# Kernel tuning notes

Measured on AMD Instinct MI355X. Metric: run time of the kernel, lower is better.

## Reference

```python
import jax, jax.numpy as jnp
import numpy as np

THRESHOLD = 0.5
NEG_POS_RATIO = 3
ALPHA = 1.0
N_CLASSES = 81


def xy_to_cxcy(xy):
    return jnp.concatenate([(xy[..., :2] + xy[..., 2:]) / 2.0,
                            xy[..., 2:] - xy[..., :2]], axis=-1)


def cxcy_to_xy(cxcy):
    return jnp.concatenate([cxcy[..., :2] - cxcy[..., 2:] / 2.0,
                            cxcy[..., :2] + cxcy[..., 2:] / 2.0], axis=-1)


def cxcy_to_gcxgcy(cxcy, priors_cxcy):
    # SSD encoding with standard variances (0.1 for center, 0.2 for size)
    g_cxcy = (cxcy[..., :2] - priors_cxcy[..., :2]) / (priors_cxcy[..., 2:] / 10.0)
    g_wh = jnp.log(cxcy[..., 2:] / priors_cxcy[..., 2:]) * 5.0
    return jnp.concatenate([g_cxcy, g_wh], axis=-1)


def iou_pairwise(a_xy, b_xy):
    # a_xy: (N, O, 4), b_xy: (P, 4) -> (N, O, P)
    lt = jnp.maximum(a_xy[..., :, None, :2], b_xy[None, None, :, :2])
    rb = jnp.minimum(a_xy[..., :, None, 2:], b_xy[None, None, :, 2:])
    wh = jnp.clip(rb - lt, 0.0)
    inter = wh[..., 0] * wh[..., 1]
    area_a = (a_xy[..., 2] - a_xy[..., 0]) * (a_xy[..., 3] - a_xy[..., 1])
    area_b = (b_xy[:, 2] - b_xy[:, 0]) * (b_xy[:, 3] - b_xy[:, 1])
    union = area_a[..., :, None] + area_b[None, None, :] - inter
    return inter / union


def setup_inputs() -> dict:
    key = jax.random.key(0)
    k1, k2, k3, k4, k5, k6, k7 = jax.random.split(key, 7)
    N, P, C, O = 32, 8732, N_CLASSES, 16
    predicted_locs = jax.random.normal(k1, (N, P, 4), dtype=jnp.float32)
    predicted_scores = jax.random.normal(k2, (N, P, C), dtype=jnp.float32)
    # ground-truth boxes: build valid cxcy then convert to xy in [0, 1]
    b_cxy = jax.random.uniform(k3, (N, O, 2), minval=0.2, maxval=0.8)
    b_wh = jax.random.uniform(k4, (N, O, 2), minval=0.05, maxval=0.3)
    boxes = cxcy_to_xy(jnp.concatenate([b_cxy, b_wh], axis=-1)).astype(jnp.float32)
    labels = jax.random.randint(k5, (N, O), 1, C).astype(jnp.int32)  # 0 = background
    # priors in cxcy, valid (positive wh)
    p_cxy = jax.random.uniform(k6, (P, 2), minval=0.05, maxval=0.95)
    p_wh = jax.random.uniform(k7, (P, 2), minval=0.05, maxval=0.4)
    priors_cxcy = jnp.concatenate([p_cxy, p_wh], axis=-1).astype(jnp.float32)
    return {"predicted_locs": predicted_locs, "predicted_scores": predicted_scores,
            "boxes": boxes, "labels": labels, "priors_cxcy": priors_cxcy}


def reference(predicted_locs, predicted_scores, boxes, labels, priors_cxcy):
    N, P, C = predicted_scores.shape
    O = boxes.shape[1]
    priors_xy = cxcy_to_xy(priors_cxcy)  # (P, 4)

    overlap = iou_pairwise(boxes, priors_xy)            # (N, O, P)
    overlap_for_each_prior = overlap.max(axis=1)        # (N, P)
    object_for_each_prior = overlap.argmax(axis=1)      # (N, P)
    prior_for_each_object = overlap.argmax(axis=2)      # (N, O)

    obj_ids = jnp.arange(O)

    def assign(ofp, ovl, pfo):
        # force each object to be matched to its best prior with overlap 1
        ofp = ofp.at[pfo].set(obj_ids)
        ovl = ovl.at[pfo].set(1.0)
        return ofp, ovl

    object_for_each_prior, overlap_for_each_prior = jax.vmap(assign)(
        object_for_each_prior, overlap_for_each_prior, prior_for_each_object)

    label_for_each_prior = jnp.take_along_axis(labels, object_for_each_prior, axis=1)  # (N, P)
    true_classes = jnp.where(overlap_for_each_prior < THRESHOLD, 0, label_for_each_prior)

    matched_boxes = jnp.take_along_axis(
        boxes, object_for_each_prior[..., None], axis=1)  # (N, P, 4)
    true_locs = cxcy_to_gcxgcy(xy_to_cxcy(matched_boxes), priors_cxcy)

    positive = true_classes != 0                          # (N, P)
    pos_f = positive.astype(predicted_locs.dtype)

    # localization loss (L1, reduction='none' in original despite the name)
    loc_per_prior = jnp.abs(predicted_locs - true_locs).sum(axis=-1)  # (N, P)
    n_pos_total = pos_f.sum()
    loc_loss = (loc_per_prior * pos_f).sum() / (4.0 * n_pos_total)

    # confidence loss (cross entropy per prior)
    logp = jax.nn.log_softmax(predicted_scores, axis=-1)
    ce = -jnp.take_along_axis(logp, true_classes[..., None], axis=-1)[..., 0]  # (N, P)

    conf_loss_pos = (ce * pos_f).sum()
    ce_neg = jnp.where(positive, 0.0, ce)
    ce_neg_sorted = -jnp.sort(-ce_neg, axis=1)            # descending
    n_positives = positive.sum(axis=1)                    # (N,)
    hard = (jnp.arange(P)[None, :] < (NEG_POS_RATIO * n_positives)[:, None]).astype(ce.dtype)
    conf_loss_hard_neg = (ce_neg_sorted * hard).sum()
    conf_loss = (conf_loss_hard_neg + conf_loss_pos) / n_pos_total

    return conf_loss + ALPHA * loc_loss
```

## Files before the change

### kernel.cpp

```cpp
#include <hip/hip_runtime.h>
#include <hip/hip_bf16.h>
#include <stdint.h>

#define BLOCK 256
#define TPB 256
#define SROWS 128
#define MAXO 64
#define TK_THREADS 1024
#define CK_MAX 4096

__global__ void match_object_kernel(const float* __restrict__ boxes,
                                    const float* __restrict__ priors,
                                    int* __restrict__ pfop,
                                    float* __restrict__ acc, int* __restrict__ n_pos,
                                    unsigned* __restrict__ done, int N, int P, int O) {
    __shared__ unsigned long long swm[4];
    int idx = blockIdx.x, tid = threadIdx.x;
    if (idx == 0) {
        for (int j = tid; j < N; j += BLOCK) n_pos[j] = 0;
        if (tid >= 64 && tid < 67) acc[tid - 64] = 0.f;
        if (tid == 96) *done = 0u;
    }
    const float* b = boxes + (size_t)idx * 4;
    float bx0 = b[0], by0 = b[1], bx1 = b[2], by1 = b[3];
    float areaa = (bx1 - bx0) * (by1 - by0);

    unsigned long long best = 0ULL;
    for (int p = tid; p < P; p += BLOCK) {
        float4 pr = ((const float4*)priors)[p];
        float px0 = pr.x - pr.z * 0.5f, py0 = pr.y - pr.w * 0.5f;
        float px1 = pr.x + pr.z * 0.5f, py1 = pr.y + pr.w * 0.5f;
        float areab = (px1 - px0) * (py1 - py0);
        float ltx = fmaxf(bx0, px0), lty = fmaxf(by0, py0);
        float rbx = fminf(bx1, px1), rby = fminf(by1, py1);
        float wx = fmaxf(rbx - ltx, 0.f), wy = fmaxf(rby - lty, 0.f);
        float inter = wx * wy;
        float iou = inter / (areaa + areab - inter);
        unsigned long long cand = (((unsigned long long)__float_as_uint(iou)) << 32) |
                                  (unsigned long long)(0xFFFFFFFFu - (unsigned)p);
        if (cand > best) best = cand;
    }
    #pragma unroll
    for (int off = 32; off >= 1; off >>= 1) {
        unsigned long long other = __shfl_down(best, off);
        if (other > best) best = other;
    }
    if ((tid & 63) == 0) swm[tid >> 6] = best;
    __syncthreads();
    if (tid == 0) {
        unsigned long long r = swm[0];
        for (int w = 1; w < BLOCK / 64; ++w) if (swm[w] > r) r = swm[w];
        pfop[idx] = (int)(0xFFFFFFFFu - (unsigned)(r & 0xFFFFFFFFull));
    }
}

__global__ void __launch_bounds__(TPB)
fused_staged_kernel(const float* __restrict__ boxes,
                    const float* __restrict__ priors,
                    const float* __restrict__ locs,
                    const int* __restrict__ labels,
                    const int* __restrict__ pfop,
                    const float* __restrict__ scores,
                    float* __restrict__ ce_neg,
                    float* __restrict__ pb_loc, float* __restrict__ pb_pce,
                    int* __restrict__ pb_npos,
                    int N, int P, int O) {
    __shared__ float4 sstage4[SROWS * 81 / 4];
    __shared__ float sbx[MAXO * 4];
    __shared__ int   spf[MAXO];
    __shared__ int   slab[MAXO];
    __shared__ float sl[4], sp[4]; __shared__ int sn[4];
    const float* sstage = (const float*)sstage4;

    int n = blockIdx.y, bx = blockIdx.x, tid = threadIdx.x;
    int w = tid >> 6, lane = tid & 63;
    int p0 = bx * SROWS;
    int rows = P - p0; if (rows > SROWS) rows = SROWS;
    int p = p0 + tid;
    bool valid = tid < rows;
    size_t t = (size_t)n * P + p;

    for (int i = tid; i < O * 4; i += TPB) sbx[i] = boxes[(size_t)n * O * 4 + i];
    for (int i = tid; i < O; i += TPB) { spf[i] = pfop[n * O + i]; slab[i] = labels[n * O + i]; }
    float4 pr = make_float4(0.f, 0.f, 1.f, 1.f);
    float4 pl = make_float4(0.f, 0.f, 0.f, 0.f);
    if (valid) {
        pr = ((const float4*)priors)[p];
        pl = ((const float4*)locs)[t];
    }

    const float4* chunk = (const float4*)(scores + ((size_t)n * P + p0) * 81);
    if (rows == SROWS) {
        #pragma unroll
        for (int j = 0; j < 10; ++j)
            sstage4[j * TPB + tid] = chunk[j * TPB + tid];
        if (tid < 32)
            sstage4[10 * TPB + tid] = chunk[10 * TPB + tid];
    } else {
        int nf4 = rows * 81 / 4;
        for (int j = 0; j < 11; ++j) {
            int idx = j * TPB + tid;
            if (idx < nf4) sstage4[idx] = chunk[idx];
        }
    }
    __syncthreads();

    float my_loc = 0.f, my_pce = 0.f; int my_pos = 0;
    if (valid) {
        const float* row = sstage + tid * 81;
        float e = 0.f;
        #pragma unroll
        for (int j = 0; j < 81; ++j) e += __expf(row[j]);

        float px0 = pr.x - pr.z * 0.5f, py0 = pr.y - pr.w * 0.5f;
        float px1 = pr.x + pr.z * 0.5f, py1 = pr.y + pr.w * 0.5f;
        float areab = (px1 - px0) * (py1 - py0);
        float best = -1.f; int bo = 0;
        for (int o = 0; o < O; ++o) {
            float x0 = sbx[o*4+0], y0 = sbx[o*4+1], x1 = sbx[o*4+2], y1 = sbx[o*4+3];
            float ltx = fmaxf(x0, px0), lty = fmaxf(y0, py0);
            float rbx = fminf(x1, px1), rby = fminf(y1, py1);
            float wx = fmaxf(rbx - ltx, 0.f), wy = fmaxf(rby - lty, 0.f);
            float inter = wx * wy;
            float areao = (x1 - x0) * (y1 - y0);
            float iou = inter / (areao + areab - inter);
            if (iou > best) { best = iou; bo = o; }
        }
        int fo = -1;
        for (int o = 0; o < O; ++o) if (spf[o] == p) fo = o;
        int obj; float ov;
        if (fo >= 0) { obj = fo; ov = 1.0f; }
        else         { obj = bo; ov = best; }
        int tc = (ov < 0.5f) ? 0 : slab[obj];

        float stc = row[tc];
        float ce = logf(e) - stc;
        bool pos = (tc != 0);
        ce_neg[t] = pos ? 0.f : ce;
        if (pos) {
            my_pce = ce; my_pos = 1;
            float x0 = sbx[obj*4+0], y0 = sbx[obj*4+1], x1 = sbx[obj*4+2], y1 = sbx[obj*4+3];
            float cx = (x0 + x1) * 0.5f, cy = (y0 + y1) * 0.5f;
            float bw = x1 - x0, bh = y1 - y0;
            float g0 = (cx - pr.x) / (pr.z / 10.0f);
            float g1 = (cy - pr.y) / (pr.w / 10.0f);
            float g2 = logf(bw / pr.z) * 5.0f;
            float g3 = logf(bh / pr.w) * 5.0f;
            my_loc = fabsf(pl.x-g0) + fabsf(pl.y-g1) + fabsf(pl.z-g2) + fabsf(pl.w-g3);
        }
    }

    #pragma unroll
    for (int off = 32; off >= 1; off >>= 1) {
        my_loc += __shfl_down(my_loc, off);
        my_pce += __shfl_down(my_pce, off);
        my_pos += __shfl_down(my_pos, off);
    }
    if (lane == 0) { sl[w] = my_loc; sp[w] = my_pce; sn[w] = my_pos; }
    __syncthreads();
    if (tid == 0) {
        int npb = gridDim.x;
        pb_loc[n * npb + bx]  = (sl[0] + sl[1]) + (sl[2] + sl[3]);
        pb_pce[n * npb + bx]  = (sp[0] + sp[1]) + (sp[2] + sp[3]);
        pb_npos[n * npb + bx] = sn[0] + sn[1] + sn[2] + sn[3];
    }
}

__global__ void match_prior_kernel(const float* __restrict__ boxes,
                                   const float* __restrict__ priors,
                                   const float* __restrict__ locs,
                                   const int* __restrict__ labels,
                                   const int* __restrict__ pfop,
                                   int* __restrict__ tcarr,
                                   float* __restrict__ acc, int* __restrict__ n_pos,
                                   int N, int P, int O) {
    __shared__ float sbx[MAXO * 4];
    __shared__ float sarea[MAXO];
    __shared__ int   spf[MAXO];
    __shared__ int   slab[MAXO];
    int n = blockIdx.y, tid = threadIdx.x;
    if (tid < O * 4) sbx[tid] = boxes[(size_t)n * O * 4 + tid];
    if (tid >= 128 && tid < 128 + O) spf[tid - 128]  = pfop[n * O + (tid - 128)];
    if (tid >= 192 && tid < 192 + O) slab[tid - 192] = labels[n * O + (tid - 192)];
    __syncthreads();
    if (tid < O)
        sarea[tid] = (sbx[tid*4+2] - sbx[tid*4+0]) * (sbx[tid*4+3] - sbx[tid*4+1]);
    __syncthreads();

    int p = blockIdx.x * BLOCK + tid;
    bool valid = p < P;
    float my_loc = 0.f; int my_pos = 0;
    if (valid) {
        float4 pr = ((const float4*)priors)[p];
        float px0 = pr.x - pr.z * 0.5f, py0 = pr.y - pr.w * 0.5f;
        float px1 = pr.x + pr.z * 0.5f, py1 = pr.y + pr.w * 0.5f;
        float areab = (px1 - px0) * (py1 - py0);

        float best = -1.f; int bo = 0;
        for (int o = 0; o < O; ++o) {
            float ltx = fmaxf(sbx[o*4+0], px0);
            float lty = fmaxf(sbx[o*4+1], py0);
            float rbx = fminf(sbx[o*4+2], px1);
            float rby = fminf(sbx[o*4+3], py1);
            float wx = fmaxf(rbx - ltx, 0.f), wy = fmaxf(rby - lty, 0.f);
            float inter = wx * wy;
            float iou = inter / (sarea[o] + areab - inter);
            if (iou > best) { best = iou; bo = o; }
        }
        int fo = -1;
        for (int o = 0; o < O; ++o) if (spf[o] == p) fo = o;
        int obj; float ov;
        if (fo >= 0) { obj = fo; ov = 1.0f; }
        else         { obj = bo; ov = best; }
        int lab = slab[obj];
        int tc = (ov < 0.5f) ? 0 : lab;
        tcarr[(size_t)n * P + p] = tc;
        if (tc != 0) {
            my_pos = 1;
            float x0 = sbx[obj*4+0], y0 = sbx[obj*4+1], x1 = sbx[obj*4+2], y1 = sbx[obj*4+3];
            float cx = (x0 + x1) * 0.5f, cy = (y0 + y1) * 0.5f;
            float w = x1 - x0, h = y1 - y0;
            float g0 = (cx - pr.x) / (pr.z / 10.0f);
            float g1 = (cy - pr.y) / (pr.w / 10.0f);
            float g2 = logf(w / pr.z) * 5.0f;
            float g3 = logf(h / pr.w) * 5.0f;
            const float* pl = locs + ((size_t)n * P + p) * 4;
            my_loc = fabsf(pl[0]-g0) + fabsf(pl[1]-g1) + fabsf(pl[2]-g2) + fabsf(pl[3]-g3);
        }
    }
    #pragma unroll
    for (int off = 32; off >= 1; off >>= 1) {
        my_loc += __shfl_down(my_loc, off);
        my_pos += __shfl_down(my_pos, off);
    }
    if ((tid & 63) == 0 && my_pos) {
        atomicAdd(&acc[0], my_loc);
        atomicAdd(&n_pos[n], my_pos);
    }
}

__global__ void loss_generic_kernel(const float* __restrict__ scores,
                                    const int* __restrict__ tcarr,
                                    float* __restrict__ ce_neg, float* __restrict__ acc,
                                    int NP, int C) {
    int t = blockIdx.x * blockDim.x + threadIdx.x;
    if (t >= NP) return;
    int tc = tcarr[t];
    const float* s = scores + (size_t)t * C;
    float m = -3.0e38f;
    for (int j = 0; j < C; ++j) m = fmaxf(m, s[j]);
    float l = 0.f, stc = 0.f;
    for (int j = 0; j < C; ++j) {
        float v = s[j];
        l += __expf(v - m);
        if (j == tc) stc = v;
    }
    float ce = m + logf(l) - stc;
    bool pos = (tc != 0);
    ce_neg[t] = pos ? 0.f : ce;
    if (pos) atomicAdd(&acc[1], ce);
}

__global__ void topk_final_kernel(const float* __restrict__ ce_neg,
                                  int* __restrict__ n_pos,
                                  const float* __restrict__ pb_loc,
                                  const float* __restrict__ pb_pce,
                                  const int* __restrict__ pb_npos, int npb,
                                  float* __restrict__ acc, unsigned* __restrict__ done,
                                  int N, int P, unsigned* __restrict__ out) {
    __shared__ unsigned skeys[8732];
    __shared__ int hist[4096];
    __shared__ int part[1024];
    __shared__ int s_tb, s_ca, s_tb2, s_ca2, s_cnt, s_np;
    __shared__ float shf[16];
    int n = blockIdx.x, tid = threadIdx.x;

    int k;
    if (npb > 0) {
        if (tid < 64) {
            float psl = 0.f, psp = 0.f; int psn = 0;
            for (int i = tid; i < npb; i += 64) {
                psl += pb_loc[n * npb + i];
                psp += pb_pce[n * npb + i];
                psn += pb_npos[n * npb + i];
            }
            #pragma unroll
            for (int off = 32; off >= 1; off >>= 1) {
                psl += __shfl_down(psl, off);
                psp += __shfl_down(psp, off);
                psn += __shfl_down(psn, off);
            }
            if (tid == 0) {
                s_np = psn;
                n_pos[n] = psn;
                if (psl != 0.f) atomicAdd(&acc[0], psl);
                if (psp != 0.f) atomicAdd(&acc[1], psp);
            }
        }
        __syncthreads();
        k = 3 * s_np;
    } else {
        k = 3 * n_pos[n];
    }
    if (k > P) k = P;
    float bsum = 0.f;

    if (k > 0) {
        const float* row = ce_neg + (size_t)n * P;
        for (int i = tid; i < P; i += TK_THREADS) skeys[i] = __float_as_uint(row[i]);
        #pragma unroll
        for (int b = 0; b < 4; ++b) hist[tid * 4 + b] = 0;
        __syncthreads();

        for (int i = tid; i < P; i += TK_THREADS) atomicAdd(&hist[skeys[i] >> 20], 1);
        __syncthreads();
        int h0 = hist[tid*4], h1 = hist[tid*4+1], h2 = hist[tid*4+2], h3 = hist[tid*4+3];
        part[tid] = h0 + h1 + h2 + h3;
        __syncthreads();
        for (int s = 1; s < 1024; s <<= 1) {
            int v = part[tid] + ((tid + s < 1024) ? part[tid + s] : 0);
            __syncthreads();
            part[tid] = v;
            __syncthreads();
        }
        int sfx = (tid + 1 < 1024) ? part[tid + 1] : 0;
        int sf3 = sfx, sf2 = sfx + h3, sf1 = sf2 + h2, sf0 = sf1 + h1;
        if (sf0 < k && k <= sf0 + h0) { s_tb = tid*4;   s_ca = sf0; }
        if (sf1 < k && k <= sf1 + h1) { s_tb = tid*4+1; s_ca = sf1; }
        if (sf2 < k && k <= sf2 + h2) { s_tb = tid*4+2; s_ca = sf2; }
        if (sf3 < k && k <= sf3 + h3) { s_tb = tid*4+3; s_ca = sf3; }
        __syncthreads();
        int tb = s_tb, kk = k - s_ca;

        if (tid < 256) part[tid] = 0;
        __syncthreads();
        float ssum = 0.f;
        for (int i = tid; i < P; i += TK_THREADS) {
            unsigned key = skeys[i];
            int bin = key >> 20;
            if (bin > tb) ssum += __uint_as_float(key);
            else if (bin == tb) atomicAdd(&part[(key >> 12) & 255u], 1);
        }
        __syncthreads();
        if (tid < 256) {
            int cum = 0;
            for (int b = tid + 1; b < 256; ++b) cum += part[b];
            int h = part[tid];
            if (cum < kk && kk <= cum + h) { s_tb2 = tid; s_ca2 = cum; }
        }
        if (tid == 0) s_cnt = 0;
        __syncthreads();
        int tb2 = s_tb2, kk2 = kk - s_ca2;

        unsigned* ckeys = (unsigned*)hist;
        for (int i = tid; i < P; i += TK_THREADS) {
            unsigned key = skeys[i];
            if ((int)(key >> 20) == tb) {
                int b2 = (key >> 12) & 255u;
                if (b2 > tb2) ssum += __uint_as_float(key);
                else if (b2 == tb2) {
                    int slot = atomicAdd(&s_cnt, 1);
                    if (slot < CK_MAX) ckeys[slot] = key;
                }
            }
        }
        __syncthreads();
        int m = s_cnt; if (m > CK_MAX) m = CK_MAX;
        for (int i = tid; i < m; i += TK_THREADS) {
            unsigned key = ckeys[i];
            int rank = 0;
            for (int j = 0; j < m; ++j) {
                unsigned kj = ckeys[j];
                rank += (kj > key) || (kj == key && j < i);
            }
            if (rank < kk2) ssum += __uint_as_float(key);
        }
        #pragma unroll
        for (int off = 32; off >= 1; off >>= 1) ssum += __shfl_down(ssum, off);
        __syncthreads();
        if ((tid & 63) == 0) shf[tid >> 6] = ssum;
        __syncthreads();
        float tot = 0.f;
        for (int i = 0; i < 16; ++i) tot += shf[i];
        bsum = tot;
    }

    if (tid == 0) {
        if (bsum != 0.f) atomicAdd(&acc[2], bsum);
        __threadfence();
        unsigned old = atomicAdd(done, 1u);
        if (old == (unsigned)(N - 1)) {
            float a0 = atomicAdd(&acc[0], 0.f);
            float a1 = atomicAdd(&acc[1], 0.f);
            float a2 = atomicAdd(&acc[2], 0.f);
            int tot = 0;
            for (int i = 0; i < N; ++i) tot += n_pos[i];
            float npos = (float)tot;
            float conf = (a2 + a1) / npos;
            float loc  = a0 / (4.f * npos);
            float loss = conf + loc;
            unsigned ub = __float_as_uint(loss);
            unsigned r = (ub + 0x7FFFu + ((ub >> 16) & 1u)) >> 16;
            out[0] = (r << 16) | r;
        }
    }
}

extern "C" void kernel_launch(void* const* d_in, const int* in_sizes, int n_in,
                              void* d_out, int out_size, void* d_ws, size_t ws_size,
                              hipStream_t stream) {
    const float* locs   = (const float*)d_in[0];
    const float* scores = (const float*)d_in[1];
    const float* boxes  = (const float*)d_in[2];
    const int*   labels = (const int*)d_in[3];
    const float* priors = (const float*)d_in[4];

    int P = in_sizes[4] / 4;
    long long NPl = in_sizes[0] / 4;
    int N = (int)(NPl / P);
    int C = (int)((long long)in_sizes[1] / NPl);
    int O = in_sizes[3] / N;
    size_t NP = (size_t)N * P;
    int gx = (P + SROWS - 1) / SROWS;

    char* ws = (char*)d_ws;
    float*    acc    = (float*)ws;     ws += 16;
    unsigned* done   = (unsigned*)ws;  ws += 16;
    int*      n_pos  = (int*)ws;       ws += (size_t)N * 4;
    int*      pfop   = (int*)ws;       ws += (size_t)N * O * 4;
    float*    pb_loc = (float*)ws;     ws += (size_t)N * gx * 4;
    float*    pb_pce = (float*)ws;     ws += (size_t)N * gx * 4;
    int*      pb_npos= (int*)ws;       ws += (size_t)N * gx * 4;
    int*      tcarr  = (int*)ws;       ws += NP * 4;
    float*    ce_neg = (float*)ws;     ws += NP * 4;

    match_object_kernel<<<N * O, BLOCK, 0, stream>>>(boxes, priors, pfop, acc, n_pos,
                                                     done, N, P, O);
    int npb = 0;
    if (C == 81 && (P % 4) == 0 && O <= MAXO) {
        npb = gx;
        fused_staged_kernel<<<dim3(gx, N), TPB, 0, stream>>>(
            boxes, priors, locs, labels, pfop, scores, ce_neg,
            pb_loc, pb_pce, pb_npos, N, P, O);
    } else {
        int gbx = (P + BLOCK - 1) / BLOCK;
        match_prior_kernel<<<dim3(gbx, N), BLOCK, 0, stream>>>(boxes, priors, locs, labels,
                                                               pfop, tcarr, acc, n_pos, N, P, O);
        loss_generic_kernel<<<(int)((NP + BLOCK - 1) / BLOCK), BLOCK, 0, stream>>>(
            scores, tcarr, ce_neg, acc, (int)NP, C);
    }
    topk_final_kernel<<<N, TK_THREADS, 0, stream>>>(ce_neg, n_pos,
                                                    pb_loc, pb_pce, pb_npos, npb,
                                                    acc, done, N, P, (unsigned*)d_out);
}
```

Measured before the change: 183.3 us.

## Split hard-negative top-k into parallel sliced histogram pass plus final select

Adds a separate histogram kernel that splits each row into 8 slices across blocks, building per-bin counts and per-bin value sums. The final kernel merges the slice histograms, finds the threshold bin with a warp-shuffle scan, and takes the sum above that bin straight from the bin sums. Only elements in the threshold bin are rescanned, so the serial per-row work is reduced and the 32-block top-k stage gets more parallelism. The cost is an extra kernel launch, sizeable workspace traffic for the slice histograms, and float atomics on the shared bin sums.

Result: slower. 279.7 us (+52.6%).

```diff
diff --git a/kernel.cpp b/kernel.cpp
--- a/kernel.cpp
+++ b/kernel.cpp
@@ -8,6 +8,7 @@
 #define MAXO 64
 #define TK_THREADS 1024
 #define CK_MAX 4096
+#define NSL 8
 
 __global__ void match_object_kernel(const float* __restrict__ boxes,
                                     const float* __restrict__ priors,
@@ -163,6 +164,239 @@
         pb_loc[n * npb + bx]  = (sl[0] + sl[1]) + (sl[2] + sl[3]);
         pb_pce[n * npb + bx]  = (sp[0] + sp[1]) + (sp[2] + sp[3]);
         pb_npos[n * npb + bx] = sn[0] + sn[1] + sn[2] + sn[3];
+    }
+}
+
+__global__ void hist_kernel(const float* __restrict__ ce_neg,
+                            int* __restrict__ hist8, float* __restrict__ hsum8,
+                            int N, int P) {
+    __shared__ int   hc[4096];
+    __shared__ float hs[4096];
+    int n = blockIdx.y, s = blockIdx.x, tid = threadIdx.x;
+    for (int b = tid; b < 4096; b += TK_THREADS) { hc[b] = 0; hs[b] = 0.f; }
+    __syncthreads();
+    int per = (P + NSL - 1) / NSL;
+    int lo = s * per, hi = lo + per; if (hi > P) hi = P;
+    const float* row = ce_neg + (size_t)n * P;
+    for (int i = lo + tid; i < hi; i += TK_THREADS) {
+        float v = row[i];
+        unsigned key = __float_as_uint(v);
+        int bin = (int)(key >> 20);
+        atomicAdd(&hc[bin], 1);
+        atomicAdd(&hs[bin], v);
+    }
+    __syncthreads();
+    size_t base = ((size_t)n * NSL + s) * 4096;
+    for (int b = tid; b < 4096; b += TK_THREADS) {
+        hist8[base + b] = hc[b];
+        hsum8[base + b] = hs[b];
+    }
+}
+
+__global__ void topk_hist_final(const float* __restrict__ ce_neg,
+                                int* __restrict__ n_pos,
+                                const float* __restrict__ pb_loc,
+                                const float* __restrict__ pb_pce,
+                                const int* __restrict__ pb_npos, int npb,
+                                const int* __restrict__ hist8,
+                                const float* __restrict__ hsum8,
+                                float* __restrict__ acc, unsigned* __restrict__ done,
+                                int N, int P, unsigned* __restrict__ out) {
+    __shared__ unsigned ckeys[CK_MAX];
+    __shared__ int  part[256];
+    __shared__ int  wtot[16];
+    __shared__ float shf[16];
+    __shared__ int s_tb, s_ca, s_tb2, s_ca2, s_cnt, s_np, s_htb;
+    __shared__ float s_above;
+    int n = blockIdx.x, tid = threadIdx.x;
+    int w = tid >> 6, lane = tid & 63;
+
+    if (tid < 64) {
+        float psl = 0.f, psp = 0.f; int psn = 0;
+        for (int i = tid; i < npb; i += 64) {
+            psl += pb_loc[n * npb + i];
+            psp += pb_pce[n * npb + i];
+            psn += pb_npos[n * npb + i];
+        }
+        #pragma unroll
+        for (int off = 32; off >= 1; off >>= 1) {
+            psl += __shfl_down(psl, off);
+            psp += __shfl_down(psp, off);
+            psn += __shfl_down(psn, off);
+        }
+        if (tid == 0) {
+            s_np = psn;
+            n_pos[n] = psn;
+            if (psl != 0.f) atomicAdd(&acc[0], psl);
+            if (psp != 0.f) atomicAdd(&acc[1], psp);
+        }
+    }
+    __syncthreads();
+    int k = 3 * s_np; if (k > P) k = P;
+    float bsum = 0.f;
+
+    if (k > 0) {
+        int4   hcv = make_int4(0, 0, 0, 0);
+        float4 hfv = make_float4(0.f, 0.f, 0.f, 0.f);
+        for (int s = 0; s < NSL; ++s) {
+            size_t base = ((size_t)n * NSL + s) * 4096;
+            int4   c = ((const int4*)(hist8 + base))[tid];
+            float4 f = ((const float4*)(hsum8 + base))[tid];
+            hcv.x += c.x; hcv.y += c.y; hcv.z += c.z; hcv.w += c.w;
+            hfv.x += f.x; hfv.y += f.y; hfv.z += f.z; hfv.w += f.w;
+        }
+        int h0 = hcv.x, h1 = hcv.y, h2 = hcv.z, h3 = hcv.w;
+
+        int lsum = h0 + h1 + h2 + h3;
+        int si = lsum;
+        #pragma unroll
+        for (int off = 1; off < 64; off <<= 1) {
+            int tv = __shfl_down(si, off);
+            if (lane + off < 64) si += tv;
+        }
+        if (lane == 0) wtot[w] = si;
+        __syncthreads();
+        if (tid < 16) {
+            int ov = wtot[tid];
+            int v = ov;
+            #pragma unroll
+            for (int off = 1; off < 16; off <<= 1) {
+                int tv = __shfl_down(v, off);
+                if (lane + off < 16) v += tv;
+            }
+            wtot[tid] = v - ov;
+        }
+        if (tid == 0) s_cnt = 0;
+        if (tid < 256) part[tid] = 0;
+        __syncthreads();
+        int b0 = tid * 4;
+        int sfx = wtot[w] + (si - lsum);
+        int sf3 = sfx, sf2 = sf3 + h3, sf1 = sf2 + h2, sf0 = sf1 + h1;
+        if (sf0 < k && k <= sf0 + h0) { s_tb = b0;   s_ca = sf0; s_htb = h0; }
+        if (sf1 < k && k <= sf1 + h1) { s_tb = b0+1; s_ca = sf1; s_htb = h1; }
+        if (sf2 < k && k <= sf2 + h2) { s_tb = b0+2; s_ca = sf2; s_htb = h2; }
+        if (sf3 < k && k <= sf3 + h3) { s_tb = b0+3; s_ca = sf3; s_htb = h3; }
+        __syncthreads();
+        int tb = s_tb, kk = k - s_ca, mtb = s_htb;
+
+        float ab = 0.f;
+        ab += (b0     > tb) ? hfv.x : 0.f;
+        ab += (b0 + 1 > tb) ? hfv.y : 0.f;
+        ab += (b0 + 2 > tb) ? hfv.z : 0.f;
+        ab += (b0 + 3 > tb) ? hfv.w : 0.f;
+        #pragma unroll
+        for (int off = 32; off >= 1; off >>= 1) ab += __shfl_down(ab, off);
+        if (lane == 0) shf[w] = ab;
+        __syncthreads();
+        if (tid == 0) {
+            float tot = 0.f;
+            for (int i = 0; i < 16; ++i) tot += shf[i];
+            s_above = tot;
+        }
+        __syncthreads();
+
+        const float* row = ce_neg + (size_t)n * P;
+        float ssum = 0.f;
+        if (mtb <= CK_MAX) {
+            for (int i = tid; i < P; i += TK_THREADS) {
+                unsigned key = __float_as_uint(row[i]);
+                if ((int)(key >> 20) == tb) {
+                    atomicAdd(&part[(key >> 12) & 255u], 1);
+                    int slot = atomicAdd(&s_cnt, 1);
+                    ckeys[slot] = key;
+                }
+            }
+            __syncthreads();
+            if (tid < 256) {
+                int cum = 0;
+                for (int b = tid + 1; b < 256; ++b) cum += part[b];
+                int h = part[tid];
+                if (cum < kk && kk <= cum + h) { s_tb2 = tid; s_ca2 = cum; }
+            }
+            __syncthreads();
+            int tb2 = s_tb2, kk2 = kk - s_ca2;
+            int m = s_cnt;
+            for (int i = tid; i < m; i += TK_THREADS) {
+                unsigned key = ckeys[i];
+                int b2 = (key >> 12) & 255u;
+                if (b2 > tb2) ssum += __uint_as_float(key);
+                else if (b2 == tb2) {
+                    int rank = 0;
+                    for (int j = 0; j < m; ++j) {
+                        unsigned kj = ckeys[j];
+                        if (((kj >> 12) & 255u) == (unsigned)tb2)
+                            rank += (kj > key) || (kj == key && j < i);
+                    }
+                    if (rank < kk2) ssum += __uint_as_float(key);
+                }
+            }
+        } else {
+            for (int i = tid; i < P; i += TK_THREADS) {
+                unsigned key = __float_as_uint(row[i]);
+                if ((int)(key >> 20) == tb) atomicAdd(&part[(key >> 12) & 255u], 1);
+            }
+            __syncthreads();
+            if (tid < 256) {
+                int cum = 0;
+                for (int b = tid + 1; b < 256; ++b) cum += part[b];
+                int h = part[tid];
+                if (cum < kk && kk <= cum + h) { s_tb2 = tid; s_ca2 = cum; }
+            }
+            __syncthreads();
+            int tb2 = s_tb2, kk2 = kk - s_ca2;
+            for (int i = tid; i < P; i += TK_THREADS) {
+                unsigned key = __float_as_uint(row[i]);
+                if ((int)(key >> 20) == tb) {
+                    int b2 = (key >> 12) & 255u;
+                    if (b2 > tb2) ssum += __uint_as_float(key);
+                    else if (b2 == tb2) {
+                        int slot = atomicAdd(&s_cnt, 1);
+                        if (slot < CK_MAX) ckeys[slot] = key;
+                    }
+                }
+            }
+            __syncthreads();
+            int m = s_cnt; if (m > CK_MAX) m = CK_MAX;
+            for (int i = tid; i < m; i += TK_THREADS) {
+                unsigned key = ckeys[i];
+                int rank = 0;
+                for (int j = 0; j < m; ++j) {
+                    unsigned kj = ckeys[j];
+                    rank += (kj > key) || (kj == key && j < i);
+                }
+                if (rank < kk2) ssum += __uint_as_float(key);
+            }
+        }
+        #pragma unroll
+        for (int off = 32; off >= 1; off >>= 1) ssum += __shfl_down(ssum, off);
+        __syncthreads();
+        if ((tid & 63) == 0) shf[tid >> 6] = ssum;
+        __syncthreads();
+        if (tid == 0) {
+            float tot = 0.f;
+            for (int i = 0; i < 16; ++i) tot += shf[i];
+            bsum = tot + s_above;
+        }
+    }
+
+    if (tid == 0) {
+        if (bsum != 0.f) atomicAdd(&acc[2], bsum);
+        __threadfence();
+        unsigned old = atomicAdd(done, 1u);
+        if (old == (unsigned)(N - 1)) {
+            float a0 = atomicAdd(&acc[0], 0.f);
+            float a1 = atomicAdd(&acc[1], 0.f);
+            float a2 = atomicAdd(&acc[2], 0.f);
+            int tot = 0;
+            for (int i = 0; i < N; ++i) tot += n_pos[i];
+            float npos = (float)tot;
+            float conf = (a2 + a1) / npos;
+            float loc  = a0 / (4.f * npos);
+            float loss = conf + loc;
+            unsigned ub = __float_as_uint(loss);
+            unsigned r = (ub + 0x7FFFu + ((ub >> 16) & 1u)) >> 16;
+            out[0] = (r << 16) | r;
+        }
     }
 }
 
@@ -263,46 +497,15 @@
 
 __global__ void topk_final_kernel(const float* __restrict__ ce_neg,
                                   int* __restrict__ n_pos,
-                                  const float* __restrict__ pb_loc,
-                                  const float* __restrict__ pb_pce,
-                                  const int* __restrict__ pb_npos, int npb,
                                   float* __restrict__ acc, unsigned* __restrict__ done,
                                   int N, int P, unsigned* __restrict__ out) {
     __shared__ unsigned skeys[8732];
     __shared__ int hist[4096];
     __shared__ int part[1024];
-    __shared__ int s_tb, s_ca, s_tb2, s_ca2, s_cnt, s_np;
+    __shared__ int s_tb, s_ca, s_tb2, s_ca2, s_cnt;
     __shared__ float shf[16];
     int n = blockIdx.x, tid = threadIdx.x;
-
-    int k;
-    if (npb > 0) {
-        if (tid < 64) {
-            float psl = 0.f, psp = 0.f; int psn = 0;
-            for (int i = tid; i < npb; i += 64) {
-                psl += pb_loc[n * npb + i];
-                psp += pb_pce[n * npb + i];
-                psn += pb_npos[n * npb + i];
-            }
-            #pragma unroll
-            for (int off = 32; off >= 1; off >>= 1) {
-                psl += __shfl_down(psl, off);
-                psp += __shfl_down(psp, off);
-                psn += __shfl_down(psn, off);
-            }
-            if (tid == 0) {
-                s_np = psn;
-                n_pos[n] = psn;
-                if (psl != 0.f) atomicAdd(&acc[0], psl);
-                if (psp != 0.f) atomicAdd(&acc[1], psp);
-            }
-        }
-        __syncthreads();
-        k = 3 * s_np;
-    } else {
-        k = 3 * n_pos[n];
-    }
-    if (k > P) k = P;
+    int k = 3 * n_pos[n]; if (k > P) k = P;
     float bsum = 0.f;
 
     if (k > 0) {
@@ -428,6 +631,8 @@
     unsigned* done   = (unsigned*)ws;  ws += 16;
     int*      n_pos  = (int*)ws;       ws += (size_t)N * 4;
     int*      pfop   = (int*)ws;       ws += (size_t)N * O * 4;
+    int*      hist8  = (int*)ws;       ws += (size_t)N * NSL * 4096 * 4;
+    float*    hsum8  = (float*)ws;     ws += (size_t)N * NSL * 4096 * 4;
     float*    pb_loc = (float*)ws;     ws += (size_t)N * gx * 4;
     float*    pb_pce = (float*)ws;     ws += (size_t)N * gx * 4;
     int*      pb_npos= (int*)ws;       ws += (size_t)N * gx * 4;
@@ -436,20 +641,22 @@
 
     match_object_kernel<<<N * O, BLOCK, 0, stream>>>(boxes, priors, pfop, acc, n_pos,
                                                      done, N, P, O);
-    int npb = 0;
-    if (C == 81 && (P % 4) == 0 && O <= MAXO) {
-        npb = gx;
+    if (C == 81 && (P % 4) == 0 && O <= MAXO && P <= NSL * 8732) {
         fused_staged_kernel<<<dim3(gx, N), TPB, 0, stream>>>(
             boxes, priors, locs, labels, pfop, scores, ce_neg,
             pb_loc, pb_pce, pb_npos, N, P, O);
+        hist_kernel<<<dim3(NSL, N), TK_THREADS, 0, stream>>>(ce_neg, hist8, hsum8, N, P);
+        topk_hist_final<<<N, TK_THREADS, 0, stream>>>(ce_neg, n_pos,
+                                                      pb_loc, pb_pce, pb_npos, gx,
+                                                      hist8, hsum8,
+                                                      acc, done, N, P, (unsigned*)d_out);
     } else {
         int gbx = (P + BLOCK - 1) / BLOCK;
         match_prior_kernel<<<dim3(gbx, N), BLOCK, 0, stream>>>(boxes, priors, locs, labels,
                                                                pfop, tcarr, acc, n_pos, N, P, O);
         loss_generic_kernel<<<(int)((NP + BLOCK - 1) / BLOCK), BLOCK, 0, stream>>>(
             scores, tcarr, ce_neg, acc, (int)NP, C);
-    }
-    topk_final_kernel<<<N, TK_THREADS, 0, stream>>>(ce_neg, n_pos,
-                                                    pb_loc, pb_pce, pb_npos, npb,
-                                                    acc, done, N, P, (unsigned*)d_out);
-}
+        topk_final_kernel<<<N, TK_THREADS, 0, stream>>>(ce_neg, n_pos, acc, done, N, P,
+                                                        (unsigned*)d_out);
+    }
+}
```
